# Optimization experiments

Measured on AMD Instinct MI355X. Metric: run time of the kernel, lower is better.

Reference implementation:

```python
import jax, jax.numpy as jnp
import numpy as np

N_NODES = 100000


def gat_conv(x, edge_index, W, att_src, att_dst, bias, concat=True, negative_slope=0.2):
    """PyG-style GATConv (eval mode, dropout off, self-loops added)."""
    N = x.shape[0]
    H, C = att_src.shape
    # add self loops (PyG default add_self_loops=True)
    ar = jnp.arange(N, dtype=edge_index.dtype)
    ei = jnp.concatenate([edge_index, jnp.stack([ar, ar])], axis=1)
    src, dst = ei[0], ei[1]

    h = (x @ W).reshape(N, H, C)                       # [N,H,C]
    a_src = (h * att_src[None]).sum(-1)                # [N,H]
    a_dst = (h * att_dst[None]).sum(-1)                # [N,H]

    e = jax.nn.leaky_relu(a_src[src] + a_dst[dst], negative_slope)  # [E,H]
    # segment softmax over destination nodes
    e_max = jax.ops.segment_max(e, dst, num_segments=N)            # [N,H]
    ex = jnp.exp(e - jax.lax.stop_gradient(e_max)[dst])
    denom = jax.ops.segment_sum(ex, dst, num_segments=N)           # [N,H]
    alpha = ex / (denom[dst] + 1e-16)                              # [E,H]

    out = jax.ops.segment_sum(alpha[:, :, None] * h[src], dst, num_segments=N)  # [N,H,C]
    out = out.reshape(N, H * C) if concat else out.mean(axis=1)
    return out + bias


def setup_inputs() -> dict:
    key = jax.random.key(0)
    ks = jax.random.split(key, 9)
    N, E, F_in, H, C = N_NODES, 3200000, 16, 4, 8
    x = jax.random.normal(ks[0], (N, F_in), dtype=jnp.float32)
    edge_index = jax.random.randint(ks[1], (2, E), 0, N, dtype=jnp.int64)
    s1 = 1.0 / np.sqrt(F_in)
    s2 = 1.0 / np.sqrt(H * C)
    return {
        "x": x,
        "edge_index": edge_index,
        "W1": jax.random.normal(ks[2], (F_in, H * C), dtype=jnp.float32) * s1,
        "att_src1": jax.random.normal(ks[3], (H, C), dtype=jnp.float32) * s2,
        "att_dst1": jax.random.normal(ks[4], (H, C), dtype=jnp.float32) * s2,
        "b1": jnp.zeros((H * C,), dtype=jnp.float32),
        "W2": jax.random.normal(ks[5], (H * C, 1), dtype=jnp.float32) * s2,
        "att_src2": jax.random.normal(ks[6], (1, 1), dtype=jnp.float32),
        "att_dst2": jax.random.normal(ks[7], (1, 1), dtype=jnp.float32),
        "b2": jnp.zeros((1,), dtype=jnp.float32),
    }


def reference(x, edge_index, W1, att_src1, att_dst1, b1, W2, att_src2, att_dst2, b2):
    h = jax.nn.elu(gat_conv(x, edge_index, W1, att_src1, att_dst1, b1, concat=True))
    return gat_conv(h, edge_index, W2, att_src2, att_dst2, b2, concat=False)
```

## Files before the change

### kernel.cpp

```cpp
#include <hip/hip_runtime.h>
#include <hip/hip_fp8.h>

#define LRELU_SLOPE 0.2f
#define BN 64
#define BSH 6
#define NC 2048
#define CAP 3840
#define TILE 8192

__device__ __forceinline__ float lrelu(float x) { return x > 0.f ? x : LRELU_SLOPE * x; }
__device__ __forceinline__ float eexp(float x)  { return __expf(fminf(x, 80.f)); }

__device__ __forceinline__ unsigned short f2bf(float f) {
    unsigned u = __float_as_uint(f);
    u += 0x7FFF + ((u >> 16) & 1);
    return (unsigned short)(u >> 16);
}
__device__ __forceinline__ float bf2f(unsigned short h) {
    return __uint_as_float((unsigned)h << 16);
}

typedef float fx2 __attribute__((ext_vector_type(2)));

#if __has_builtin(__builtin_amdgcn_cvt_pk_f32_fp8) && __has_builtin(__builtin_amdgcn_cvt_pk_fp8_f32)
#define HW_FP8 1
#else
#define HW_FP8 0
#endif

__device__ __forceinline__ void fp8x8_to_f32(unsigned rx, unsigned ry, float* o) {
#if HW_FP8
    fx2 a = __builtin_amdgcn_cvt_pk_f32_fp8((int)rx, false);
    fx2 b = __builtin_amdgcn_cvt_pk_f32_fp8((int)rx, true);
    fx2 c = __builtin_amdgcn_cvt_pk_f32_fp8((int)ry, false);
    fx2 d = __builtin_amdgcn_cvt_pk_f32_fp8((int)ry, true);
    o[0]=a.x; o[1]=a.y; o[2]=b.x; o[3]=b.y;
    o[4]=c.x; o[5]=c.y; o[6]=d.x; o[7]=d.y;
#else
#pragma unroll
    for (int i = 0; i < 8; ++i) {
        unsigned bb = (i < 4 ? rx : ry) >> ((i & 3) * 8);
        unsigned em = bb & 0x7F;
        float f = (em >= 8) ? __uint_as_float((em << 20) + 0x3C000000u)
                            : (float)em * 0.001953125f;
        o[i] = (bb & 0x80) ? -f : f;
    }
#endif
}

__device__ __forceinline__ unsigned f32x4_to_fp8(float a, float b, float c, float d) {
#if HW_FP8
    int w = __builtin_amdgcn_cvt_pk_fp8_f32(a, b, 0, false);
    w = __builtin_amdgcn_cvt_pk_fp8_f32(c, d, w, true);
    return (unsigned)w;
#else
    __hip_fp8_e4m3 qa(a), qb(b), qc(c), qd(d);
    return (unsigned)qa.__x | ((unsigned)qb.__x << 8) |
           ((unsigned)qc.__x << 16) | ((unsigned)qd.__x << 24);
#endif
}

__global__ __launch_bounds__(256) void kA(
    const float* __restrict__ x, const float* __restrict__ W1,
    const float* __restrict__ att_src1, const float* __restrict__ att_dst1,
    unsigned char* __restrict__ rec, float* __restrict__ ad1,
    const int* __restrict__ dst, int* __restrict__ hist,
    int N, int E, int nbn)
{
    __shared__ float sW[512];
    __shared__ float sAs[32], sAd[32];
    __shared__ int hl[NC];
    int tid = threadIdx.x;

    if ((int)blockIdx.x >= nbn) {
        int blk = blockIdx.x - nbn;
        for (int i = tid; i < NC; i += 256) hl[i] = 0;
        __syncthreads();
        int e0 = blk * TILE, e1 = min(e0 + TILE, E);
        for (int e = e0 + tid; e < e1; e += 256)
            atomicAdd(&hl[dst[e] >> BSH], 1);
        __syncthreads();
        for (int i = tid; i < NC; i += 256)
            hist[(size_t)blk * NC + i] = hl[i];
        return;
    }

    for (int i = tid; i < 512; i += 256) sW[i] = W1[i];
    if (tid < 32) { sAs[tid] = att_src1[tid]; sAd[tid] = att_dst1[tid]; }
    __syncthreads();
    int n = blockIdx.x * 256 + tid;
    if (n >= N) return;

    float xr[16];
    const float4* xp = (const float4*)(x + (size_t)n * 16);
    float4 v0 = xp[0], v1 = xp[1], v2 = xp[2], v3 = xp[3];
    xr[0]=v0.x; xr[1]=v0.y; xr[2]=v0.z;  xr[3]=v0.w;
    xr[4]=v1.x; xr[5]=v1.y; xr[6]=v1.z;  xr[7]=v1.w;
    xr[8]=v2.x; xr[9]=v2.y; xr[10]=v2.z; xr[11]=v2.w;
    xr[12]=v3.x;xr[13]=v3.y;xr[14]=v3.z; xr[15]=v3.w;

    float h[32];
#pragma unroll
    for (int j = 0; j < 32; ++j) {
        float acc = 0.f;
#pragma unroll
        for (int i = 0; i < 16; ++i) acc = fmaf(xr[i], sW[i * 32 + j], acc);
        h[j] = acc;
    }

    float asr[4], adr[4];
#pragma unroll
    for (int hh = 0; hh < 4; ++hh) {
        float as = 0.f, ad = 0.f;
#pragma unroll
        for (int c = 0; c < 8; ++c) {
            as = fmaf(h[hh * 8 + c], sAs[hh * 8 + c], as);
            ad = fmaf(h[hh * 8 + c], sAd[hh * 8 + c], ad);
        }
        asr[hh] = as; adr[hh] = ad;
    }

    unsigned w0[4], w1[4], w2[4];
#pragma unroll
    for (int hh = 0; hh < 4; ++hh) {
        w0[hh] = f32x4_to_fp8(h[8*hh+0], h[8*hh+1], h[8*hh+2], h[8*hh+3]);
        w1[hh] = f32x4_to_fp8(h[8*hh+4], h[8*hh+5], h[8*hh+6], h[8*hh+7]);
        w2[hh] = (unsigned)f2bf(asr[hh]);
    }
    uint4* rp = (uint4*)(rec + (size_t)n * 48);
    rp[0] = make_uint4(w0[0], w1[0], w2[0], w0[1]);
    rp[1] = make_uint4(w1[1], w2[1], w0[2], w1[2]);
    rp[2] = make_uint4(w2[2], w0[3], w1[3], w2[3]);

    *(float4*)(ad1 + (size_t)n * 4) = make_float4(adr[0], adr[1], adr[2], adr[3]);
}

__global__ __launch_bounds__(256) void kscan(
    const int* __restrict__ hist, int* __restrict__ histoff,
    int* __restrict__ bukcnt, int NBLK)
{
    __shared__ int sm[256 * 17];
    int tid = threadIdx.x;
    int c0 = blockIdx.x * 16;
    int carry[16];
#pragma unroll
    for (int i = 0; i < 16; ++i) carry[i] = 0;
    int* myrow = sm + tid * 17;

    for (int base = 0; base < NBLK; base += 256) {
        int idx = base + tid;
        int v[16], own[16];
        if (idx < NBLK) {
            const int4* rp = (const int4*)(hist + (size_t)idx * NC + c0);
            int4 a = rp[0], b = rp[1], c = rp[2], d = rp[3];
            v[0]=a.x; v[1]=a.y; v[2]=a.z;  v[3]=a.w;
            v[4]=b.x; v[5]=b.y; v[6]=b.z;  v[7]=b.w;
            v[8]=c.x; v[9]=c.y; v[10]=c.z; v[11]=c.w;
            v[12]=d.x; v[13]=d.y; v[14]=d.z; v[15]=d.w;
        } else {
#pragma unroll
            for (int i = 0; i < 16; ++i) v[i] = 0;
        }
#pragma unroll
        for (int i = 0; i < 16; ++i) { own[i] = v[i]; myrow[i] = v[i]; }
        __syncthreads();
        for (int off = 1; off < 256; off <<= 1) {
            int t[16];
            if (tid >= off) {
                const int* nb = sm + (tid - off) * 17;
#pragma unroll
                for (int i = 0; i < 16; ++i) t[i] = nb[i];
            } else {
#pragma unroll
                for (int i = 0; i < 16; ++i) t[i] = 0;
            }
            __syncthreads();
#pragma unroll
            for (int i = 0; i < 16; ++i) { v[i] += t[i]; myrow[i] = v[i]; }
            __syncthreads();
        }
        if (idx < NBLK) {
            int4* wp = (int4*)(histoff + (size_t)idx * NC + c0);
            int e[16];
#pragma unroll
            for (int i = 0; i < 16; ++i) e[i] = carry[i] + v[i] - own[i];
            wp[0] = make_int4(e[0], e[1], e[2], e[3]);
            wp[1] = make_int4(e[4], e[5], e[6], e[7]);
            wp[2] = make_int4(e[8], e[9], e[10], e[11]);
            wp[3] = make_int4(e[12], e[13], e[14], e[15]);
        }
        const int* last = sm + 255 * 17;
#pragma unroll
        for (int i = 0; i < 16; ++i) carry[i] += last[i];
        __syncthreads();
    }
    if (tid == 0) {
        int4* bp = (int4*)(bukcnt + c0);
        bp[0] = make_int4(carry[0], carry[1], carry[2], carry[3]);
        bp[1] = make_int4(carry[4], carry[5], carry[6], carry[7]);
        bp[2] = make_int4(carry[8], carry[9], carry[10], carry[11]);
        bp[3] = make_int4(carry[12], carry[13], carry[14], carry[15]);
    }
}

__global__ __launch_bounds__(256) void kscanB(
    const int* __restrict__ bukcnt, int* __restrict__ bukoff)
{
    __shared__ int sd[256];
    int tid = threadIdx.x;
    int4 a = ((const int4*)bukcnt)[2 * tid];
    int4 c = ((const int4*)bukcnt)[2 * tid + 1];
    int tsum = a.x + a.y + a.z + a.w + c.x + c.y + c.z + c.w;
    sd[tid] = tsum; __syncthreads();
    for (int off = 1; off < 256; off <<= 1) {
        int t = (tid >= off) ? sd[tid - off] : 0; __syncthreads();
        sd[tid] += t; __syncthreads();
    }
    int excl = sd[tid] - tsum;
    int4 oa, ob;
    oa.x = excl;        oa.y = oa.x + a.x; oa.z = oa.y + a.y; oa.w = oa.z + a.z;
    ob.x = oa.w + a.w;  ob.y = ob.x + c.x; ob.z = ob.y + c.y; ob.w = ob.z + c.z;
    ((int4*)bukoff)[2 * tid] = oa;
    ((int4*)bukoff)[2 * tid + 1] = ob;
}

#define KP2_BST (TILE * 4)
#define KP2_CUR (KP2_BST + ((NC + 1) * 2 + 2))
#define KP2_LDS (KP2_CUR + NC * 4)

__global__ __launch_bounds__(512) void kpass2(
    const int* __restrict__ src, const int* __restrict__ dst,
    const int* __restrict__ hist, const int* __restrict__ histoff,
    const int* __restrict__ bukoff,
    unsigned* __restrict__ ebuk, int E)
{
    __shared__ __align__(16) unsigned char smem[KP2_LDS];
    unsigned* staged = (unsigned*)smem;
    unsigned short* bstart = (unsigned short*)(smem + KP2_BST);
    int* cur = (int*)(smem + KP2_CUR);
    int* partial = (int*)smem;

    int tid = threadIdx.x, blk = blockIdx.x;
    int4 c4 = ((const int4*)(hist + (size_t)blk * NC))[tid];
    int tsum = c4.x + c4.y + c4.z + c4.w;
    partial[tid] = tsum;
    __syncthreads();
    for (int off = 1; off < 512; off <<= 1) {
        int t = (tid >= off) ? partial[tid - off] : 0; __syncthreads();
        partial[tid] += t; __syncthreads();
    }
    int excl = partial[tid] - tsum;
    int b4 = tid * 4;
    int e0v = excl, e1v = excl + c4.x, e2v = e1v + c4.y, e3v = e2v + c4.z;
    cur[b4] = e0v; cur[b4+1] = e1v; cur[b4+2] = e2v; cur[b4+3] = e3v;
    bstart[b4]   = (unsigned short)e0v;
    bstart[b4+1] = (unsigned short)e1v;
    bstart[b4+2] = (unsigned short)e2v;
    bstart[b4+3] = (unsigned short)e3v;
    if (tid == 511) bstart[NC] = (unsigned short)(e3v + c4.w);
    __syncthreads();

    int e0 = blk * TILE, e1 = min(e0 + TILE, E);
    for (int e = e0 + tid; e < e1; e += 512) {
        int s = src[e], d = dst[e];
        int b = d >> BSH;
        int pos = atomicAdd(&cur[b], 1);
        staged[pos] = ((unsigned)(d & (BN - 1)) << 17) | (unsigned)s;
    }
    __syncthreads();

    for (int b = tid; b < NC; b += 512) {
        int p0 = bstart[b], p1 = bstart[b + 1];
        int gb = bukoff[b] + histoff[(size_t)blk * NC + b];
        for (int p = p0; p < p1; ++p)
            ebuk[gb + (p - p0)] = staged[p];
    }
}

__global__ __launch_bounds__(256, 6) void ksort_agg1(
    unsigned* __restrict__ ebuk, const int* __restrict__ bukoff,
    const unsigned char* __restrict__ rec, const float* __restrict__ ad1,
    const float* __restrict__ b1, const float* __restrict__ W2,
    float* __restrict__ h2, int* __restrict__ rowptr, int N)
{
    __shared__ int sbuf[CAP];
    __shared__ int cnt[BN], exc[BN], cur[BN];
    __shared__ float sb[32], sw[32];
    int tid = threadIdx.x;
    int b = blockIdx.x;
    int n0 = b << BSH;
    int r0 = bukoff[b], r1 = bukoff[b + 1];
    int tot = r1 - r0;

    if (tid < 32) { sb[tid] = b1[tid]; sw[tid] = W2[tid]; }
    if (tid < BN) cnt[tid] = 0;
    __syncthreads();

    for (int i = tid; i < tot; i += 256)
        atomicAdd(&cnt[ebuk[r0 + i] >> 17], 1);
    __syncthreads();

    if (tid < BN) exc[tid] = cnt[tid];
    __syncthreads();
    for (int off = 1; off < BN; off <<= 1) {
        int t = 0;
        if (tid < BN && tid >= off) t = exc[tid - off];
        __syncthreads();
        if (tid < BN) exc[tid] += t;
        __syncthreads();
    }
    if (tid < BN) {
        int e = exc[tid] - cnt[tid];
        exc[tid] = e;
        cur[tid] = e;
        int n = n0 + tid;
        if (n <= N) rowptr[n] = r0 + e;
    }
    __syncthreads();

    for (int i = tid; i < tot; i += 256) {
        unsigned pk = ebuk[r0 + i];
        int dl = pk >> 17;
        int pos = atomicAdd(&cur[dl], 1);
        if (pos < CAP) sbuf[pos] = (int)(pk & 0x1FFFF);
    }
    __syncthreads();
    for (int i = tid; i < tot; i += 256)
        ebuk[r0 + i] = (unsigned)sbuf[min(i, CAP - 1)];

    int g = tid >> 2, l = tid & 3;
    {
        int dl = g;
        int n = n0 + dl;
        if (n < N) {
            float adh = ad1[(size_t)n * 4 + l];
            uint3 rs = *(const uint3*)(rec + (size_t)n * 48 + l * 12);
            float ass = bf2f((unsigned short)(rs.z & 0xFFFF));
            float wself = eexp(lrelu(ass + adh));
            float dsum = wself;
            float acc[8], hv[8];
            fp8x8_to_f32(rs.x, rs.y, hv);
#pragma unroll
            for (int ch = 0; ch < 8; ++ch) acc[ch] = wself * hv[ch];

            int p0 = exc[dl];
            int p1 = min(p0 + cnt[dl], CAP);
            int p = p0;
            for (; p + 8 <= p1; p += 8) {
                int sidx[8];
                uint3 uv[8];
#pragma unroll
                for (int q = 0; q < 8; ++q) sidx[q] = sbuf[p + q];
#pragma unroll
                for (int q = 0; q < 8; ++q)
                    uv[q] = *(const uint3*)(rec + (size_t)sidx[q] * 48 + l * 12);
#pragma unroll
                for (int q = 0; q < 8; ++q) {
                    float ash = bf2f((unsigned short)(uv[q].z & 0xFFFF));
                    float w = eexp(lrelu(ash + adh));
                    float sv[8];
                    fp8x8_to_f32(uv[q].x, uv[q].y, sv);
                    dsum += w;
#pragma unroll
                    for (int ch = 0; ch < 8; ++ch)
                        acc[ch] = fmaf(w, sv[ch], acc[ch]);
                }
            }
            for (; p < p1; ++p) {
                int s = sbuf[p];
                uint3 r = *(const uint3*)(rec + (size_t)s * 48 + l * 12);
                float ash = bf2f((unsigned short)(r.z & 0xFFFF));
                float sv[8];
                fp8x8_to_f32(r.x, r.y, sv);
                float w = eexp(lrelu(ash + adh));
                dsum += w;
#pragma unroll
                for (int ch = 0; ch < 8; ++ch)
                    acc[ch] = fmaf(w, sv[ch], acc[ch]);
            }
            float inv = 1.f / (dsum + 1e-16f);
            float partial = 0.f;
#pragma unroll
            for (int ch = 0; ch < 8; ++ch) {
                float o = fmaf(acc[ch], inv, sb[l * 8 + ch]);
                o = o > 0.f ? o : __expf(o) - 1.f;
                partial = fmaf(o, sw[l * 8 + ch], partial);
            }
            partial += __shfl_xor(partial, 1);
            partial += __shfl_xor(partial, 2);
            if (l == 0) h2[n] = partial;
        }
    }
}

__global__ __launch_bounds__(256) void kagg2(
    const unsigned* __restrict__ esrc, const int* __restrict__ rowptr,
    const float* __restrict__ h2,
    const float* __restrict__ att_src2, const float* __restrict__ att_dst2,
    const float* __restrict__ b2, float* __restrict__ out, int N)
{
    int tid = threadIdx.x;
    int g = tid >> 3, l = tid & 7;
    int n = blockIdx.x * 32 + g;
    if (n >= N) return;
    float s2 = att_src2[0], d2 = att_dst2[0];
    int r0 = rowptr[n], r1 = rowptr[n + 1];
    float h2d = h2[n];
    float add = h2d * d2;
    float den = 0.f, acc = 0.f;
    if (l == 0) {
        float ws = eexp(lrelu(fmaf(h2d, s2, add)));
        den = ws; acc = ws * h2d;
    }
    int p = r0 + l;
    for (; p + 8 < r1; p += 16) {
        int s0 = (int)esrc[p], s1 = (int)esrc[p + 8];
        float ha = h2[s0], hb = h2[s1];
        float wa = eexp(lrelu(fmaf(ha, s2, add)));
        float wb = eexp(lrelu(fmaf(hb, s2, add)));
        den += wa + wb;
        acc = fmaf(wa, ha, acc);
        acc = fmaf(wb, hb, acc);
    }
    if (p < r1) {
        int s = (int)esrc[p];
        float hs = h2[s];
        float w = eexp(lrelu(fmaf(hs, s2, add)));
        den += w;
        acc = fmaf(w, hs, acc);
    }
    den += __shfl_xor(den, 1); acc += __shfl_xor(acc, 1);
    den += __shfl_xor(den, 2); acc += __shfl_xor(acc, 2);
    den += __shfl_xor(den, 4); acc += __shfl_xor(acc, 4);
    if (l == 0) out[n] = acc / (den + 1e-16f) + b2[0];
}

extern "C" void kernel_launch(void* const* d_in, const int* in_sizes, int n_in,
                              void* d_out, int out_size, void* d_ws, size_t ws_size,
                              hipStream_t stream)
{
    const float* x        = (const float*)d_in[0];
    const int*   ei       = (const int*)d_in[1];
    const float* W1       = (const float*)d_in[2];
    const float* att_src1 = (const float*)d_in[3];
    const float* att_dst1 = (const float*)d_in[4];
    const float* b1       = (const float*)d_in[5];
    const float* W2       = (const float*)d_in[6];
    const float* att_src2 = (const float*)d_in[7];
    const float* att_dst2 = (const float*)d_in[8];
    const float* b2       = (const float*)d_in[9];

    const int N = in_sizes[0] / 16;
    const int E = in_sizes[1] / 2;
    const int* src = ei;
    const int* dst = ei + E;

    const int NBUK = (N + BN - 1) >> BSH;
    const int NBLK = (E + TILE - 1) / TILE;
    const int nb_n = (N + 255) / 256;

    unsigned char* rec = (unsigned char*)d_ws;
    float* ad1   = (float*)(rec + (size_t)N * 48);
    float* h2    = ad1 + (size_t)N * 4;
    int* rowptr  = (int*)(h2 + N);
    int* bukcnt  = rowptr + N + 64;
    int* bukoff  = bukcnt + NC;
    int* hist    = bukoff + NC;
    int* histoff = hist + (size_t)NBLK * NC;
    unsigned* ebuk = (unsigned*)(histoff + (size_t)NBLK * NC);

    kA<<<nb_n + NBLK, 256, 0, stream>>>(x, W1, att_src1, att_dst1,
                                        rec, ad1, dst, hist,
                                        N, E, nb_n);
    kscan<<<NC / 16, 256, 0, stream>>>(hist, histoff, bukcnt, NBLK);
    kscanB<<<1, 256, 0, stream>>>(bukcnt, bukoff);
    kpass2<<<NBLK, 512, 0, stream>>>(src, dst, hist, histoff, bukoff, ebuk, E);
    ksort_agg1<<<NBUK, 256, 0, stream>>>(ebuk, bukoff, rec, ad1,
                                         b1, W2, h2, rowptr, N);
    kagg2<<<(N + 31) / 32, 256, 0, stream>>>(ebuk, rowptr, h2,
                                             att_src2, att_dst2,
                                             b2, (float*)d_out, N);
}
```

Measured before the change: 192.2 us.

## Aggregate layer 2 directly from bucketed edges with LDS atomics, drop CSR writeback

Layer-1 aggregation no longer writes the locally sorted source list and row pointers back to global memory. Layer 2 now runs one block per 64-node bucket, reads the packed (dst-local, src) bucket entries directly, and accumulates the softmax numerator and denominator per node with shared-memory float atomics. This removes a 3.2M-entry global write plus the rowptr array. In exchange it adds LDS atomic contention, and the float summation order becomes nondeterministic.

```diff
diff --git a/kernel.cpp b/kernel.cpp
--- a/kernel.cpp
+++ b/kernel.cpp
@@ -278,10 +278,10 @@
 }
 
 __global__ __launch_bounds__(256, 6) void ksort_agg1(
-    unsigned* __restrict__ ebuk, const int* __restrict__ bukoff,
+    const unsigned* __restrict__ ebuk, const int* __restrict__ bukoff,
     const unsigned char* __restrict__ rec, const float* __restrict__ ad1,
     const float* __restrict__ b1, const float* __restrict__ W2,
-    float* __restrict__ h2, int* __restrict__ rowptr, int N)
+    float* __restrict__ h2, int N)
 {
     __shared__ int sbuf[CAP];
     __shared__ int cnt[BN], exc[BN], cur[BN];
@@ -313,8 +313,6 @@
         int e = exc[tid] - cnt[tid];
         exc[tid] = e;
         cur[tid] = e;
-        int n = n0 + tid;
-        if (n <= N) rowptr[n] = r0 + e;
     }
     __syncthreads();
 
@@ -325,8 +323,6 @@
         if (pos < CAP) sbuf[pos] = (int)(pk & 0x1FFFF);
     }
     __syncthreads();
-    for (int i = tid; i < tot; i += 256)
-        ebuk[r0 + i] = (unsigned)sbuf[min(i, CAP - 1)];
 
     int g = tid >> 2, l = tid & 3;
     {
@@ -394,45 +390,45 @@
 }
 
 __global__ __launch_bounds__(256) void kagg2(
-    const unsigned* __restrict__ esrc, const int* __restrict__ rowptr,
+    const unsigned* __restrict__ ebuk, const int* __restrict__ bukoff,
     const float* __restrict__ h2,
     const float* __restrict__ att_src2, const float* __restrict__ att_dst2,
     const float* __restrict__ b2, float* __restrict__ out, int N)
 {
+    __shared__ float h2L[BN], den[BN], acc[BN];
     int tid = threadIdx.x;
-    int g = tid >> 3, l = tid & 7;
-    int n = blockIdx.x * 32 + g;
-    if (n >= N) return;
+    int b = blockIdx.x;
+    int n0 = b << BSH;
     float s2 = att_src2[0], d2 = att_dst2[0];
-    int r0 = rowptr[n], r1 = rowptr[n + 1];
-    float h2d = h2[n];
-    float add = h2d * d2;
-    float den = 0.f, acc = 0.f;
-    if (l == 0) {
-        float ws = eexp(lrelu(fmaf(h2d, s2, add)));
-        den = ws; acc = ws * h2d;
-    }
-    int p = r0 + l;
-    for (; p + 8 < r1; p += 16) {
-        int s0 = (int)esrc[p], s1 = (int)esrc[p + 8];
-        float ha = h2[s0], hb = h2[s1];
-        float wa = eexp(lrelu(fmaf(ha, s2, add)));
-        float wb = eexp(lrelu(fmaf(hb, s2, add)));
-        den += wa + wb;
-        acc = fmaf(wa, ha, acc);
-        acc = fmaf(wb, hb, acc);
-    }
-    if (p < r1) {
-        int s = (int)esrc[p];
+
+    if (tid < BN) {
+        int n = n0 + tid;
+        if (n < N) {
+            float hv = h2[n];
+            h2L[tid] = hv;
+            float w = eexp(lrelu(hv * s2 + hv * d2));
+            den[tid] = w;
+            acc[tid] = w * hv;
+        } else { h2L[tid] = 0.f; den[tid] = 0.f; acc[tid] = 0.f; }
+    }
+    __syncthreads();
+
+    int r0 = bukoff[b], r1 = bukoff[b + 1];
+    for (int p = r0 + tid; p < r1; p += 256) {
+        unsigned pk = ebuk[p];
+        int s  = (int)(pk & 0x1FFFF);
+        int dl = (int)(pk >> 17);
         float hs = h2[s];
-        float w = eexp(lrelu(fmaf(hs, s2, add)));
-        den += w;
-        acc = fmaf(w, hs, acc);
-    }
-    den += __shfl_xor(den, 1); acc += __shfl_xor(acc, 1);
-    den += __shfl_xor(den, 2); acc += __shfl_xor(acc, 2);
-    den += __shfl_xor(den, 4); acc += __shfl_xor(acc, 4);
-    if (l == 0) out[n] = acc / (den + 1e-16f) + b2[0];
+        float w = eexp(lrelu(fmaf(hs, s2, h2L[dl] * d2)));
+        atomicAdd(&den[dl], w);
+        atomicAdd(&acc[dl], w * hs);
+    }
+    __syncthreads();
+
+    if (tid < BN) {
+        int n = n0 + tid;
+        if (n < N) out[n] = acc[tid] / (den[tid] + 1e-16f) + b2[0];
+    }
 }
 
 extern "C" void kernel_launch(void* const* d_in, const int* in_sizes, int n_in,
@@ -462,8 +458,7 @@
     unsigned char* rec = (unsigned char*)d_ws;
     float* ad1   = (float*)(rec + (size_t)N * 48);
     float* h2    = ad1 + (size_t)N * 4;
-    int* rowptr  = (int*)(h2 + N);
-    int* bukcnt  = rowptr + N + 64;
+    int* bukcnt  = (int*)(h2 + N);
     int* bukoff  = bukcnt + NC;
     int* hist    = bukoff + NC;
     int* histoff = hist + (size_t)NBLK * NC;
@@ -476,8 +471,7 @@
     kscanB<<<1, 256, 0, stream>>>(bukcnt, bukoff);
     kpass2<<<NBLK, 512, 0, stream>>>(src, dst, hist, histoff, bukoff, ebuk, E);
     ksort_agg1<<<NBUK, 256, 0, stream>>>(ebuk, bukoff, rec, ad1,
-                                         b1, W2, h2, rowptr, N);
-    kagg2<<<(N + 31) / 32, 256, 0, stream>>>(ebuk, rowptr, h2,
-                                             att_src2, att_dst2,
-                                             b2, (float*)d_out, N);
-}
+                                         b1, W2, h2, N);
+    kagg2<<<NBUK, 256, 0, stream>>>(ebuk, bukoff, h2, att_src2, att_dst2,
+                                    b2, (float*)d_out, N);
+}
```

Measured after the change: 209.4 us. +8.9%, slower.
